# Optimization experiments

Hardware: AMD Instinct MI355X
Metric: run time of the kernel (lower is better)

The kernel has to match this reference:

```python
import jax, jax.numpy as jnp
import numpy as np

NUM_HEADS = 12
DIM_HEAD = 32
EMBED_DIM = NUM_HEADS * DIM_HEAD  # 384
EPS = 1e-5


def _channel_layernorm(x, w, b):
    # LayerNorm over channel axis (axis=1) of [B, D, S, L], per spatial position
    mu = jnp.mean(x, axis=1, keepdims=True)
    var = jnp.mean(jnp.square(x - mu), axis=1, keepdims=True)
    xn = (x - mu) / jnp.sqrt(var + EPS)
    return xn * w[None, :, None, None] + b[None, :, None, None]


def _qkv(x, w, b):
    # 1x1 conv == per-position matmul: [3D, D] x [B, D, S, L] -> [B, 3D, S, L]
    B, D, S, L = x.shape
    y = jnp.einsum('od,bdsl->bosl', w, x) + b[None, :, None, None]
    q, k, v = jnp.split(y, 3, axis=1)
    shp = (B, NUM_HEADS, DIM_HEAD, S, L)
    return q.reshape(shp), k.reshape(shp), v.reshape(shp)


def setup_inputs() -> dict:
    key = jax.random.key(0)
    ks = jax.random.split(key, 5)
    B, D, S, L = 1, EMBED_DIM, 128, 256
    x = jax.random.normal(ks[0], (B, D, S, L), dtype=jnp.float32)
    row_w = jax.random.normal(ks[1], (3 * D, D), dtype=jnp.float32) * (D ** -0.5)
    row_b = jax.random.normal(ks[2], (3 * D,), dtype=jnp.float32) * 0.02
    col_w = jax.random.normal(ks[3], (3 * D, D), dtype=jnp.float32) * (D ** -0.5)
    col_b = jax.random.normal(ks[4], (3 * D,), dtype=jnp.float32) * 0.02
    return {
        'x': x,
        'row_w': row_w, 'row_b': row_b,
        'col_w': col_w, 'col_b': col_b,
        'ln1_w': jnp.ones((D,), jnp.float32), 'ln1_b': jnp.zeros((D,), jnp.float32),
        'ln2_w': jnp.ones((D,), jnp.float32), 'ln2_b': jnp.zeros((D,), jnp.float32),
    }


def reference(x, row_w, row_b, col_w, col_b, ln1_w, ln1_b, ln2_w, ln2_b):
    B, D, S, L = x.shape
    # --- row attention (attend across L within each row s) ---
    q, k, v = _qkv(x, row_w, row_b)  # [B,H,C,S,L]
    row_attn = jnp.einsum('bhcsi,bhcsj->bhsij', q, k)  # note: no 1/sqrt(d) scaling (faithful)
    row_attn = jax.nn.softmax(row_attn, axis=-1)
    row_out = jnp.einsum('bhsij,bhdsj->bhdsi', row_attn, v).reshape(B, D, S, L)
    out = _channel_layernorm(x + row_out, ln1_w, ln1_b)
    # --- column attention (attend across S within each column l) ---
    q, k, v = _qkv(out, col_w, col_b)
    col_attn = jnp.einsum('bhcil,bhcjl->bhijl', q, k)
    col_attn = jax.nn.softmax(col_attn, axis=-2)
    col_out = jnp.einsum('bhijl,bhdjl->bhdil', col_attn, v).reshape(B, D, S, L)
    out = _channel_layernorm(out + col_out, ln2_w, ln2_b)
    return out
```

## Files before the change

kernel.cpp:

```cpp
#include <hip/hip_runtime.h>
#include <math.h>

#define DCH 384
#define NH 12
#define CH 32
#define SS 128
#define LL 256
#define NPOS 32768
#define THREE_D 1152

typedef _Float16 f16_t;
typedef _Float16 f16x4 __attribute__((ext_vector_type(4)));
typedef _Float16 f16x8 __attribute__((ext_vector_type(8)));
typedef float f32x4 __attribute__((ext_vector_type(4)));

#define GLD16(gptr, lptr) __builtin_amdgcn_global_load_lds( \
    (const __attribute__((address_space(1))) unsigned int*)(gptr), \
    (__attribute__((address_space(3))) unsigned int*)(lptr), 16, 0, 0)

#define WAVE_LDS_FENCE() __asm__ volatile("s_waitcnt lgkmcnt(0)" ::: "memory")

__global__ __launch_bounds__(256) void conv_w(const float* __restrict__ in,
                                              f16_t* __restrict__ out, int n4) {
    int i = blockIdx.x * 256 + threadIdx.x;
    if (i < n4) {
        float4 v = ((const float4*)in)[i];
        unsigned short u0 = __builtin_bit_cast(unsigned short, (f16_t)v.x);
        unsigned short u1 = __builtin_bit_cast(unsigned short, (f16_t)v.y);
        unsigned short u2 = __builtin_bit_cast(unsigned short, (f16_t)v.z);
        unsigned short u3 = __builtin_bit_cast(unsigned short, (f16_t)v.w);
        uint2 r;
        r.x = (unsigned)u0 | ((unsigned)u1 << 16);
        r.y = (unsigned)u2 | ((unsigned)u3 << 16);
        ((uint2*)out)[i] = r;
    }
}

__global__ __launch_bounds__(256) void conv_xT(const float* __restrict__ in,
                                               f16_t* __restrict__ outp) {
    __shared__ float tile[64][65];
    const int p0 = blockIdx.x * 64;
    const int k0 = blockIdx.y * 64;
    const int tx = threadIdx.x & 63, ty = threadIdx.x >> 6;
#pragma unroll
    for (int i = 0; i < 16; ++i)
        tile[ty * 16 + i][tx] = in[(size_t)(k0 + ty * 16 + i) * NPOS + p0 + tx];
    __syncthreads();
    const int pr = threadIdx.x >> 2;
    const int cg = threadIdx.x & 3;
    union { uint4 v[2]; unsigned int u[8]; } res;
#pragma unroll
    for (int j = 0; j < 8; ++j) {
        unsigned short lo = __builtin_bit_cast(unsigned short, (f16_t)tile[cg * 16 + 2 * j][pr]);
        unsigned short hi = __builtin_bit_cast(unsigned short, (f16_t)tile[cg * 16 + 2 * j + 1][pr]);
        res.u[j] = (unsigned)lo | ((unsigned)hi << 16);
    }
    uint4* dst = (uint4*)&outp[(size_t)(p0 + pr) * DCH + k0 + cg * 16];
    dst[0] = res.v[0];
    dst[1] = res.v[1];
}

__global__ __launch_bounds__(256) void qkv_gemm_f16(
        const f16_t* __restrict__ Wh,
        const float* __restrict__ bias,
        const f16_t* __restrict__ Xp,
        f16_t* __restrict__ Yq, f16_t* __restrict__ Yk, f16_t* __restrict__ Yv)
{
    __shared__ f16_t sha[128 * 32];
    __shared__ f16_t shb[128 * 32];
    const int tid  = threadIdx.x;
    const int lane = tid & 63;
    const int wave = tid >> 6;
    const int ot   = blockIdx.x;
    const int o0 = ot * 128;
    const int p0 = blockIdx.y * 128;
    const int wr = wave >> 1, wc = wave & 1;

    f32x4 acc[4][4] = {};

    const int c0 = wave * 128 + lane;
    const int c1 = c0 + 64;
    const f16_t* ga0 = Wh + (size_t)(o0 + (c0 >> 2)) * DCH + (c0 & 3) * 8;
    const f16_t* ga1 = Wh + (size_t)(o0 + (c1 >> 2)) * DCH + (c1 & 3) * 8;
    const f16_t* gb0 = Xp + (size_t)(p0 + (c0 >> 2)) * DCH + (c0 & 3) * 8;
    const f16_t* gb1 = Xp + (size_t)(p0 + (c1 >> 2)) * DCH + (c1 & 3) * 8;
    f16_t* la0 = sha + (wave * 128) * 8;
    f16_t* la1 = sha + (wave * 128 + 64) * 8;
    f16_t* lb0 = shb + (wave * 128) * 8;
    f16_t* lb1 = shb + (wave * 128 + 64) * 8;

    const int mrow = lane & 15;
    const int kg8  = (lane >> 4) * 8;

    for (int kk = 0; kk < DCH; kk += 32) {
        GLD16(ga0 + kk, la0);
        GLD16(ga1 + kk, la1);
        GLD16(gb0 + kk, lb0);
        GLD16(gb1 + kk, lb1);
        __syncthreads();
        f16x8 af[4], bfr[4];
#pragma unroll
        for (int mi = 0; mi < 4; ++mi)
            af[mi] = *(const f16x8*)(sha + (wr * 64 + mi * 16 + mrow) * 32 + kg8);
#pragma unroll
        for (int ni = 0; ni < 4; ++ni)
            bfr[ni] = *(const f16x8*)(shb + (wc * 64 + ni * 16 + mrow) * 32 + kg8);
#pragma unroll
        for (int mi = 0; mi < 4; ++mi)
#pragma unroll
            for (int ni = 0; ni < 4; ++ni)
                acc[mi][ni] = __builtin_amdgcn_mfma_f32_16x16x32_f16(
                    af[mi], bfr[ni], acc[mi][ni], 0, 0, 0);
        __syncthreads();
    }

    const int col = lane & 15;
    const int rq4 = (lane >> 4) * 4;
    const int qkv = ot / 3;
    const int grp = ot % 3;

    if (qkv < 2) {
        f16_t* Yt = (qkv == 0) ? Yq : Yk;
#pragma unroll
        for (int mi = 0; mi < 4; ++mi) {
            const int h  = grp * 4 + wr * 2 + (mi >> 1);
            const int cb = (mi & 1) * 16 + rq4;
            const int ob = o0 + wr * 64 + mi * 16 + rq4;
            const float b0 = bias[ob], b1 = bias[ob + 1];
            const float b2 = bias[ob + 2], b3 = bias[ob + 3];
#pragma unroll
            for (int ni = 0; ni < 4; ++ni) {
                const int p = p0 + wc * 64 + ni * 16 + col;
                union { uint2 u; f16_t h4[4]; } w;
                w.h4[0] = (f16_t)(acc[mi][ni][0] + b0);
                w.h4[1] = (f16_t)(acc[mi][ni][1] + b1);
                w.h4[2] = (f16_t)(acc[mi][ni][2] + b2);
                w.h4[3] = (f16_t)(acc[mi][ni][3] + b3);
                *(uint2*)(Yt + ((size_t)h * NPOS + p) * CH + cb) = w.u;
            }
        }
    } else {
#pragma unroll
        for (int mi = 0; mi < 4; ++mi) {
#pragma unroll
            for (int r = 0; r < 4; ++r) {
                const int cg = grp * 128 + wr * 64 + mi * 16 + rq4 + r;
                const float br = bias[768 + cg];
#pragma unroll
                for (int ni = 0; ni < 4; ++ni) {
                    const int p = p0 + wc * 64 + ni * 16 + col;
                    Yv[(size_t)cg * NPOS + p] = (f16_t)(acc[mi][ni][r] + br);
                }
            }
        }
    }
}

template <int SEQ, bool XT16>
__global__ __launch_bounds__(256) void mfma_attn(
        const f16_t* __restrict__ Yq, const f16_t* __restrict__ Yk,
        const f16_t* __restrict__ Yv, const void* __restrict__ Xv_,
        float* __restrict__ R)
{
    constexpr int JT  = SEQ / 16;
    constexpr int NIT = SEQ / 64;
    constexpr int PST = SEQ + 8;
    __shared__ f16_t pb[4][16 * PST];
    const int lane = threadIdx.x & 63;
    const int wave = threadIdx.x >> 6;
    const int col = lane & 15, quad = lane >> 4;
    const int h = blockIdx.x % NH;
    const size_t pbase = (size_t)(blockIdx.x / NH) * SEQ;

    const f16_t* qg = Yq + ((size_t)h * NPOS + pbase) * CH;
    const f16_t* kg = Yk + ((size_t)h * NPOS + pbase) * CH;
    const f16_t* vg = Yv + (size_t)h * CH * NPOS + pbase;
    f16_t* mypb = pb[wave];

    for (int it = 0; it < NIT; ++it) {
        const int i0 = (wave * NIT + it) * 16;
        const f16x8 qf = *(const f16x8*)(qg + (size_t)(i0 + col) * CH + quad * 8);
        f32x4 st[JT];
#pragma unroll
        for (int mt = 0; mt < JT; ++mt) {
            f16x8 kf = *(const f16x8*)(kg + (size_t)(mt * 16 + col) * CH + quad * 8);
            st[mt] = __builtin_amdgcn_mfma_f32_16x16x32_f16(kf, qf, (f32x4){0.f, 0.f, 0.f, 0.f}, 0, 0, 0);
        }
        float sum = 0.f;
#pragma unroll
        for (int mt = 0; mt < JT; ++mt)
#pragma unroll
            for (int r = 0; r < 4; ++r) {
                st[mt][r] = __expf(st[mt][r]);
                sum += st[mt][r];
            }
        sum += __shfl_xor(sum, 16, 64);
        sum += __shfl_xor(sum, 32, 64);
        const float inv = 1.f / sum;
#pragma unroll
        for (int mt = 0; mt < JT; ++mt) {
            union { uint2 u; f16_t h4[4]; } w;
            w.h4[0] = (f16_t)(st[mt][0] * inv);
            w.h4[1] = (f16_t)(st[mt][1] * inv);
            w.h4[2] = (f16_t)(st[mt][2] * inv);
            w.h4[3] = (f16_t)(st[mt][3] * inv);
            *(uint2*)(mypb + col * PST + mt * 16 + quad * 4) = w.u;
        }
        WAVE_LDS_FENCE();

        f32x4 ot0 = {0.f, 0.f, 0.f, 0.f}, ot1 = {0.f, 0.f, 0.f, 0.f};
#pragma unroll
        for (int ks = 0; ks < SEQ / 32; ++ks) {
            f16x8 pf = *(const f16x8*)(mypb + col * PST + ks * 32 + quad * 8);
            f16x8 v0 = *(const f16x8*)(vg + (size_t)col * NPOS + ks * 32 + quad * 8);
            f16x8 v1 = *(const f16x8*)(vg + (size_t)(16 + col) * NPOS + ks * 32 + quad * 8);
            ot0 = __builtin_amdgcn_mfma_f32_16x16x32_f16(v0, pf, ot0, 0, 0, 0);
            ot1 = __builtin_amdgcn_mfma_f32_16x16x32_f16(v1, pf, ot1, 0, 0, 0);
        }
        const size_t pos = pbase + i0 + col;
        if constexpr (XT16) {
            const f16_t* Xh = (const f16_t*)Xv_;
            const f16x4 xa = *(const f16x4*)(Xh + pos * DCH + h * CH + quad * 4);
            const f16x4 xb = *(const f16x4*)(Xh + pos * DCH + h * CH + 16 + quad * 4);
#pragma unroll
            for (int r = 0; r < 4; ++r) {
                R[(size_t)(h * CH + quad * 4 + r) * NPOS + pos]      = (float)xa[r] + ot0[r];
                R[(size_t)(h * CH + 16 + quad * 4 + r) * NPOS + pos] = (float)xb[r] + ot1[r];
            }
        } else {
            const float* Xf = (const float*)Xv_;
#pragma unroll
            for (int r = 0; r < 4; ++r) {
                const size_t c0r = (size_t)(h * CH + quad * 4 + r) * NPOS + pos;
                const size_t c1r = (size_t)(h * CH + 16 + quad * 4 + r) * NPOS + pos;
                R[c0r] = Xf[c0r] + ot0[r];
                R[c1r] = Xf[c1r] + ot1[r];
            }
        }
    }
}

__global__ __launch_bounds__(256) void ln_stats(const float* __restrict__ A,
                                                float* __restrict__ mu,
                                                float* __restrict__ rs) {
    __shared__ float ssum[4][64], ssq[4][64];
    const int i = threadIdx.x & 63;
    const int g = threadIdx.x >> 6;
    const int p = blockIdx.x * 64 + i;
    float sum = 0.f, sq = 0.f;
    const float* ap = A + (size_t)(g * 96) * NPOS + p;
#pragma unroll 4
    for (int d = 0; d < 96; ++d) {
        float v = ap[(size_t)d * NPOS];
        sum += v;
        sq += v * v;
    }
    ssum[g][i] = sum;
    ssq[g][i] = sq;
    __syncthreads();
    if (g == 0) {
        float s = ssum[0][i] + ssum[1][i] + ssum[2][i] + ssum[3][i];
        float q = ssq[0][i] + ssq[1][i] + ssq[2][i] + ssq[3][i];
        float m = s * (1.f / DCH);
        float var = q * (1.f / DCH) - m * m;
        mu[p] = m;
        rs[p] = rsqrtf(var + 1e-5f);
    }
}

__global__ __launch_bounds__(256) void norm_xT(
        const float* __restrict__ A, const float* __restrict__ mu,
        const float* __restrict__ rs, const float* __restrict__ w,
        const float* __restrict__ b, f16_t* __restrict__ Xp) {
    __shared__ float tile[64][65];
    const int l0 = (blockIdx.x & 3) * 64;
    const int s  = (blockIdx.x >> 2) & (SS - 1);
    const int k0 = (blockIdx.x >> 9) * 64;
    const int tx = threadIdx.x & 63, ty = threadIdx.x >> 6;
    const int pos0 = s * LL + l0;
#pragma unroll
    for (int i = 0; i < 16; ++i) {
        const int d = k0 + ty * 16 + i;
        float v = A[(size_t)d * NPOS + pos0 + tx];
        tile[ty * 16 + i][tx] = (v - mu[pos0 + tx]) * rs[pos0 + tx] * w[d] + b[d];
    }
    __syncthreads();
    const int pr = threadIdx.x >> 2;
    const int cg = threadIdx.x & 3;
    union { uint4 v[2]; unsigned int u[8]; } res;
#pragma unroll
    for (int j = 0; j < 8; ++j) {
        unsigned short lo = __builtin_bit_cast(unsigned short, (f16_t)tile[cg * 16 + 2 * j][pr]);
        unsigned short hi = __builtin_bit_cast(unsigned short, (f16_t)tile[cg * 16 + 2 * j + 1][pr]);
        res.u[j] = (unsigned)lo | ((unsigned)hi << 16);
    }
    uint4* dst = (uint4*)&Xp[(size_t)((l0 + pr) * SS + s) * DCH + k0 + cg * 16];
    dst[0] = res.v[0];
    dst[1] = res.v[1];
}

__global__ __launch_bounds__(256) void norm_transpose(
        const float* __restrict__ in, const float* __restrict__ mu,
        const float* __restrict__ rs, const float* __restrict__ w,
        const float* __restrict__ b, float* __restrict__ out, int Rr, int Cc) {
    __shared__ float tile[32][33];
    const int ntc = Cc >> 5, ntr = Rr >> 5;
    int tc = blockIdx.x % ntc;
    int tr = (blockIdx.x / ntc) % ntr;
    int d = blockIdx.x / (ntc * ntr);
    int tx = threadIdx.x & 31, ty = threadIdx.x >> 5;
    const float* ip = in + (size_t)d * Rr * Cc;
    float* op = out + (size_t)d * Rr * Cc;
    const float wd = w[d], bd = b[d];
#pragma unroll
    for (int i = 0; i < 32; i += 8) {
        const int r = tr * 32 + ty + i;
        const int c = tc * 32 + tx;
        const int pos = r * Cc + c;
        float v = ip[(size_t)r * Cc + c];
        tile[ty + i][tx] = (v - mu[pos]) * rs[pos] * wd + bd;
    }
    __syncthreads();
#pragma unroll
    for (int i = 0; i < 32; i += 8)
        op[(size_t)(tc * 32 + ty + i) * Rr + tr * 32 + tx] = tile[tx][ty + i];
}

extern "C" void kernel_launch(void* const* d_in, const int* in_sizes, int n_in,
                              void* d_out, int out_size, void* d_ws, size_t ws_size,
                              hipStream_t stream) {
    const float* x     = (const float*)d_in[0];
    const float* row_w = (const float*)d_in[1];
    const float* row_b = (const float*)d_in[2];
    const float* col_w = (const float*)d_in[3];
    const float* col_b = (const float*)d_in[4];
    const float* ln1_w = (const float*)d_in[5];
    const float* ln1_b = (const float*)d_in[6];
    const float* ln2_w = (const float*)d_in[7];
    const float* ln2_b = (const float*)d_in[8];
    float* out = (float*)d_out;

    char* ws = (char*)d_ws;
    const size_t ysz = (size_t)NH * NPOS * CH * 2;
    const size_t abytes = (size_t)DCH * NPOS * 4;
    f16_t* Yq = (f16_t*)ws;
    f16_t* Yk = (f16_t*)(ws + ysz);
    f16_t* Yv = (f16_t*)(ws + 2 * ysz);
    float* A  = (float*)(ws + 3 * ysz);
    f16_t* Xp = (f16_t*)(ws + 3 * ysz + abytes);
    f16_t* Wh = (f16_t*)(ws + 3 * ysz + abytes + ysz);
    float* MU = (float*)(ws + 3 * ysz + abytes + ysz + (1 << 21));
    float* RS = MU + NPOS;

    dim3 ggrid(THREE_D / 128, NPOS / 128);
    const int wn4 = THREE_D * DCH / 4;
    dim3 cgrid(NPOS / 64, DCH / 64);

    conv_w<<<(wn4 + 255) / 256, 256, 0, stream>>>(row_w, Wh, wn4);
    conv_xT<<<cgrid, 256, 0, stream>>>(x, Xp);
    qkv_gemm_f16<<<ggrid, 256, 0, stream>>>(Wh, row_b, Xp, Yq, Yk, Yv);
    mfma_attn<LL, false><<<NH * SS, 256, 0, stream>>>(Yq, Yk, Yv, x, A);
    ln_stats<<<NPOS / 64, 256, 0, stream>>>(A, MU, RS);
    norm_xT<<<(DCH / 64) * SS * (LL / 64), 256, 0, stream>>>(A, MU, RS, ln1_w, ln1_b, Xp);

    conv_w<<<(wn4 + 255) / 256, 256, 0, stream>>>(col_w, Wh, wn4);
    qkv_gemm_f16<<<ggrid, 256, 0, stream>>>(Wh, col_b, Xp, Yq, Yk, Yv);
    mfma_attn<SS, true><<<NH * LL, 256, 0, stream>>>(Yq, Yk, Yv, Xp, A);
    ln_stats<<<NPOS / 64, 256, 0, stream>>>(A, MU, RS);
    norm_transpose<<<DCH * (LL / 32) * (SS / 32), 256, 0, stream>>>(
        A, MU, RS, ln2_w, ln2_b, out, LL, SS);
}
```

Baseline: 394.4 us.

## Stage K and V tiles in LDS for attention and split PV accumulators

The attention kernel now loads each block's K tile into shared memory with direct global-to-LDS loads and copies the V tile into padded shared memory, behind a block barrier. All four waves then read K and V from LDS instead of reloading them from global memory on every iteration. The PV loop also keeps two independent accumulator chains per output tile to give the MFMA units more instruction-level parallelism. In exchange the kernel uses more LDS, which may lower occupancy, and adds a synchronization point before compute starts.

```diff
diff --git a/kernel.cpp b/kernel.cpp
--- a/kernel.cpp
+++ b/kernel.cpp
@@ -165,9 +165,13 @@
     constexpr int JT  = SEQ / 16;
     constexpr int NIT = SEQ / 64;
     constexpr int PST = SEQ + 8;
+    constexpr int VST = SEQ + 8;
+    __shared__ f16_t Ks[SEQ * CH];
+    __shared__ f16_t Vs[CH * VST];
     __shared__ f16_t pb[4][16 * PST];
-    const int lane = threadIdx.x & 63;
-    const int wave = threadIdx.x >> 6;
+    const int tid  = threadIdx.x;
+    const int lane = tid & 63;
+    const int wave = tid >> 6;
     const int col = lane & 15, quad = lane >> 4;
     const int h = blockIdx.x % NH;
     const size_t pbase = (size_t)(blockIdx.x / NH) * SEQ;
@@ -177,13 +181,29 @@
     const f16_t* vg = Yv + (size_t)h * CH * NPOS + pbase;
     f16_t* mypb = pb[wave];
 
+#pragma unroll
+    for (int i = 0; i < SEQ / 64; ++i) {
+        const int off = (wave * (SEQ / 64) + i) * 512;
+        GLD16(kg + off + lane * 8, Ks + off);
+    }
+    {
+        constexpr int CPR = SEQ / 8;
+        const int vch = tid % CPR;
+        const int vr0 = tid / CPR;
+#pragma unroll
+        for (int r = vr0; r < CH; r += 256 / CPR)
+            *(float4*)(Vs + r * VST + vch * 8) =
+                *(const float4*)(vg + (size_t)r * NPOS + vch * 8);
+    }
+    __syncthreads();
+
     for (int it = 0; it < NIT; ++it) {
         const int i0 = (wave * NIT + it) * 16;
         const f16x8 qf = *(const f16x8*)(qg + (size_t)(i0 + col) * CH + quad * 8);
         f32x4 st[JT];
 #pragma unroll
         for (int mt = 0; mt < JT; ++mt) {
-            f16x8 kf = *(const f16x8*)(kg + (size_t)(mt * 16 + col) * CH + quad * 8);
+            f16x8 kf = *(const f16x8*)(Ks + (mt * 16 + col) * CH + quad * 8);
             st[mt] = __builtin_amdgcn_mfma_f32_16x16x32_f16(kf, qf, (f32x4){0.f, 0.f, 0.f, 0.f}, 0, 0, 0);
         }
         float sum = 0.f;
@@ -208,15 +228,24 @@
         }
         WAVE_LDS_FENCE();
 
-        f32x4 ot0 = {0.f, 0.f, 0.f, 0.f}, ot1 = {0.f, 0.f, 0.f, 0.f};
-#pragma unroll
-        for (int ks = 0; ks < SEQ / 32; ++ks) {
-            f16x8 pf = *(const f16x8*)(mypb + col * PST + ks * 32 + quad * 8);
-            f16x8 v0 = *(const f16x8*)(vg + (size_t)col * NPOS + ks * 32 + quad * 8);
-            f16x8 v1 = *(const f16x8*)(vg + (size_t)(16 + col) * NPOS + ks * 32 + quad * 8);
-            ot0 = __builtin_amdgcn_mfma_f32_16x16x32_f16(v0, pf, ot0, 0, 0, 0);
-            ot1 = __builtin_amdgcn_mfma_f32_16x16x32_f16(v1, pf, ot1, 0, 0, 0);
-        }
+        f32x4 o0a = {0.f, 0.f, 0.f, 0.f}, o0b = {0.f, 0.f, 0.f, 0.f};
+        f32x4 o1a = {0.f, 0.f, 0.f, 0.f}, o1b = {0.f, 0.f, 0.f, 0.f};
+#pragma unroll
+        for (int ks = 0; ks < SEQ / 32; ks += 2) {
+            f16x8 pf0 = *(const f16x8*)(mypb + col * PST + ks * 32 + quad * 8);
+            f16x8 pf1 = *(const f16x8*)(mypb + col * PST + (ks + 1) * 32 + quad * 8);
+            f16x8 va0 = *(const f16x8*)(Vs + col * VST + ks * 32 + quad * 8);
+            f16x8 va1 = *(const f16x8*)(Vs + col * VST + (ks + 1) * 32 + quad * 8);
+            f16x8 vb0 = *(const f16x8*)(Vs + (16 + col) * VST + ks * 32 + quad * 8);
+            f16x8 vb1 = *(const f16x8*)(Vs + (16 + col) * VST + (ks + 1) * 32 + quad * 8);
+            o0a = __builtin_amdgcn_mfma_f32_16x16x32_f16(va0, pf0, o0a, 0, 0, 0);
+            o0b = __builtin_amdgcn_mfma_f32_16x16x32_f16(va1, pf1, o0b, 0, 0, 0);
+            o1a = __builtin_amdgcn_mfma_f32_16x16x32_f16(vb0, pf0, o1a, 0, 0, 0);
+            o1b = __builtin_amdgcn_mfma_f32_16x16x32_f16(vb1, pf1, o1b, 0, 0, 0);
+        }
+        const f32x4 ot0 = o0a + o0b;
+        const f32x4 ot1 = o1a + o1b;
+
         const size_t pos = pbase + i0 + col;
         if constexpr (XT16) {
             const f16_t* Xh = (const f16_t*)Xv_;
```

New measurement: 366.5 us. 7.1% less time.
